# Kernel optimization log

Measured on AMD Instinct MI355X. Metric: run time of the kernel, lower is better.

Reference implementation:

```python
import jax, jax.numpy as jnp
import numpy as np

# ---- architecture constants ----
SENSOR = 128          # u feature width
B_LAYERS = 5          # branch MLP: 4 tanh hidden + 1 linear out
B_UNITS = 1024
LORA = 64
TU = 128              # trunk hidden units
TL = 4                # trunk dense layers
TRUNK_DIMS = [1] + [TU] * (TL - 1) + [1]   # 1 -> 128 -> 128 -> 128 -> 1
NO_TRUNK_PARAMS = sum(d_out + d_in * d_out for d_in, d_out in zip(TRUNK_DIMS[:-1], TRUNK_DIMS[1:]))  # 33409
T0, TFINAL = 0.0, 1.0
BATCH = 2048


def setup_inputs() -> dict:
    key = jax.random.key(0)
    ks = jax.random.split(key, 16)
    def glorot(k, shape):
        fan_in, fan_out = shape[0], shape[1]
        s = jnp.sqrt(2.0 / (fan_in + fan_out)).astype(jnp.float32)
        return jax.random.normal(k, shape, dtype=jnp.float32) * s
    inp = {
        "t": jax.random.uniform(ks[0], (BATCH, 1), dtype=jnp.float32),
        "u": jax.random.normal(ks[1], (BATCH, SENSOR), dtype=jnp.float32),
        # branch MLP: Dense(1024)+tanh x4, then Dense(1024)
        "bw0": glorot(ks[2], (SENSOR, B_UNITS)), "bb0": jnp.zeros((B_UNITS,), jnp.float32),
        "bw1": glorot(ks[3], (B_UNITS, B_UNITS)), "bb1": jnp.zeros((B_UNITS,), jnp.float32),
        "bw2": glorot(ks[4], (B_UNITS, B_UNITS)), "bb2": jnp.zeros((B_UNITS,), jnp.float32),
        "bw3": glorot(ks[5], (B_UNITS, B_UNITS)), "bb3": jnp.zeros((B_UNITS,), jnp.float32),
        "bw4": glorot(ks[6], (B_UNITS, B_UNITS)), "bb4": jnp.zeros((B_UNITS,), jnp.float32),
        # LoRA factors generating trunk params
        "W1": glorot(ks[7], (B_UNITS, LORA)),
        "W2": glorot(ks[8], (LORA, NO_TRUNK_PARAMS)),
    }
    return inp


def _slice_trunk(p):
    """Split per-sample flat trunk params [B,P] into (kernel,bias) per layer.
    Flax tree_flatten order per Dense: bias then kernel."""
    layers = []
    k = 0
    for d_in, d_out in zip(TRUNK_DIMS[:-1], TRUNK_DIMS[1:]):
        b = p[:, k:k + d_out]; k += d_out
        W = p[:, k:k + d_in * d_out].reshape(-1, d_in, d_out); k += d_in * d_out
        layers.append((W, b))
    return layers


def reference(t, u, bw0, bb0, bw1, bb1, bw2, bb2, bw3, bb3, bw4, bb4, W1, W2):
    q0 = u[:, :1]                                     # [B,1]
    # branch MLP (hypernetwork body)
    net = u
    for W, b in ((bw0, bb0), (bw1, bb1), (bw2, bb2), (bw3, bb3)):
        net = jnp.tanh(net @ W + b)
    net = net @ bw4 + bb4                             # [B, units]
    # LoRA-generated per-sample trunk params
    params = net @ (W1 @ W2)                          # [B, NO_TRUNK_PARAMS]
    # batched per-sample trunk MLP on t[i] (vectorized form of the Python loop)
    x = t                                             # [B,1]
    trunk_layers = _slice_trunk(params)
    for i, (W, b) in enumerate(trunk_layers):
        x = jnp.einsum('bi,bio->bo', x, W) + b
        if i < TL - 1:
            x = jnp.tanh(x)
    q = x                                             # [B,1]
    # hard constraint: u0 + (t-t0)/(tfinal-t0)*nn
    out = q0 + (t - T0) / (TFINAL - T0) * q           # [B,1]
    return out.reshape(-1)
```

## Files before the change

### kernel.cpp

```cpp
#include <hip/hip_runtime.h>
#include <hip/hip_bf16.h>
#include <stdint.h>

typedef unsigned short u16;
typedef unsigned int   u32;
typedef short s16x8 __attribute__((ext_vector_type(8)));
typedef float f32x4 __attribute__((ext_vector_type(4)));

#define LDP 33409

__device__ __forceinline__ u16 f2bf(float f) {
    union { float f; u32 u; } v; v.f = f;
    u32 r = v.u + 0x7fffu + ((v.u >> 16) & 1u);
    return (u16)(r >> 16);
}
__device__ __forceinline__ float bf2f(u16 h) {
    union { u32 u; float f; } v; v.u = ((u32)h) << 16;
    return v.f;
}
__device__ __forceinline__ float fast_tanh(float x) {
    float e = __expf(2.0f * x);
    return 1.0f - 2.0f / (e + 1.0f);
}
__device__ __forceinline__ f32x4 MFMA(s16x8 a, s16x8 b, f32x4 c) {
    return __builtin_amdgcn_mfma_f32_16x16x32_bf16(a, b, c, 0, 0, 0);
}
__device__ __forceinline__ void gload_lds16(const void* g, void* l) {
    __builtin_amdgcn_global_load_lds(
        (const __attribute__((address_space(1))) u32*)(uintptr_t)g,
        (__attribute__((address_space(3))) u32*)(uintptr_t)l, 16, 0, 0);
}

__global__ __launch_bounds__(256)
void prep0(const float* __restrict__ u, const float* __restrict__ bw0,
           u16* __restrict__ ubf, u16* __restrict__ bw0t)
{
    __shared__ float tile[64][65];
    const int bid = blockIdx.x, tid = threadIdx.x;
    if (bid < 128) {
        int i = (bid * 256 + tid) * 8;
        float4 a = *(const float4*)&u[i];
        float4 b = *(const float4*)&u[i + 4];
        uint4 o;
        o.x = (u32)f2bf(a.x) | ((u32)f2bf(a.y) << 16);
        o.y = (u32)f2bf(a.z) | ((u32)f2bf(a.w) << 16);
        o.z = (u32)f2bf(b.x) | ((u32)f2bf(b.y) << 16);
        o.w = (u32)f2bf(b.z) | ((u32)f2bf(b.w) << 16);
        *(uint4*)&ubf[i] = o;
        return;
    }
    const int idx = bid - 128;
    const int rb = (idx >> 4) * 64, cb = (idx & 15) * 64;
    for (int i = tid; i < 64 * 64; i += 256) {
        int r = i >> 6, c = i & 63;
        tile[r][c] = bw0[(size_t)(rb + r) * 1024 + cb + c];
    }
    __syncthreads();
    for (int i = tid; i < 64 * 64; i += 256) {
        int c = i >> 6, r = i & 63;
        bw0t[(size_t)(cb + c) * 128 + rb + r] = f2bf(tile[r][c]);
    }
}

__global__ __launch_bounds__(256, 2)
void gemm_fused(const u16* __restrict__ A, int lda,
                const u16* __restrict__ Bt, int ldb,
                const float* __restrict__ bias,
                u16* __restrict__ Cout, int ldc, int K, int mode,
                const float* __restrict__ xsrc, u16* __restrict__ xdst,
                const float* __restrict__ bw4, const float* __restrict__ bb4,
                const float* __restrict__ W1, u16* __restrict__ BWt,
                float* __restrict__ bz,
                const float* __restrict__ W2, u16* __restrict__ Btb)
{
    __shared__ __align__(16) char lds[16640];
    const int bid = blockIdx.x, tid = threadIdx.x;

    if (bid < 512) {
        u16 (*As)[64 * 32] = (u16(*)[64 * 32])lds;
        u16 (*Bs)[64 * 32] = (u16(*)[64 * 32])(lds + 8192);
        const int lane = tid & 63, wid = tid >> 6;
        const int wr = wid >> 1, wc = wid & 1;
        const int bn = (bid & 15) * 64, bm = (bid >> 4) * 64;
        const int NT = K >> 5;
        const int arow = tid >> 2, ck = tid & 3;
        const u16* aSrc = A + (size_t)(bm + arow) * lda + (ck ^ (arow & 3)) * 8;
        const u16* bSrc = Bt + (size_t)(bn + arow) * ldb + (ck ^ (arow & 3)) * 8;
        f32x4 acc[2][2] = {};

        auto STAGE = [&](int buf, int t) {
            const int k0 = t << 5;
            gload_lds16(aSrc + k0, (char*)As[buf] + wid * 1024);
            gload_lds16(bSrc + k0, (char*)Bs[buf] + wid * 1024);
        };
        auto COMPUTE = [&](int buf) {
            s16x8 a[2], b[2];
            #pragma unroll
            for (int mi = 0; mi < 2; ++mi) {
                int row = wr * 32 + mi * 16 + (lane & 15);
                int s = (lane >> 4) ^ (row & 3);
                a[mi] = *(const s16x8*)&As[buf][row * 32 + s * 8];
            }
            #pragma unroll
            for (int ni = 0; ni < 2; ++ni) {
                int n = wc * 32 + ni * 16 + (lane & 15);
                int s = (lane >> 4) ^ (n & 3);
                b[ni] = *(const s16x8*)&Bs[buf][n * 32 + s * 8];
            }
            #pragma unroll
            for (int mi = 0; mi < 2; ++mi)
            #pragma unroll
            for (int ni = 0; ni < 2; ++ni)
                acc[mi][ni] = MFMA(a[mi], b[ni], acc[mi][ni]);
        };

        STAGE(0, 0);
        __syncthreads();
        for (int t = 0; t < NT; ++t) {
            if (t + 1 < NT) STAGE((t + 1) & 1, t + 1);
            COMPUTE(t & 1);
            __syncthreads();
        }
        #pragma unroll
        for (int mi = 0; mi < 2; ++mi)
        #pragma unroll
        for (int ni = 0; ni < 2; ++ni) {
            const int col = bn + wc * 32 + ni * 16 + (lane & 15);
            const float bv = bias[col];
            #pragma unroll
            for (int jj = 0; jj < 4; ++jj) {
                const int row = bm + wr * 32 + mi * 16 + (lane >> 4) * 4 + jj;
                Cout[(size_t)row * ldc + col] = f2bf(fast_tanh(acc[mi][ni][jj] + bv));
            }
        }
    } else if (mode <= 2 && bid < 768) {
        float (*tile)[65] = (float(*)[65])lds;
        const int idx = bid - 512;
        const int rb = (idx >> 4) * 64, cb = (idx & 15) * 64;
        for (int i = tid; i < 64 * 64; i += 256) {
            int r = i >> 6, c = i & 63;
            tile[r][c] = xsrc[(size_t)(rb + r) * 1024 + cb + c];
        }
        __syncthreads();
        for (int i = tid; i < 64 * 64; i += 256) {
            int c = i >> 6, r = i & 63;
            xdst[(size_t)(cb + c) * 1024 + rb + r] = f2bf(tile[r][c]);
        }
    } else if (mode == 2) {
        const int lb = bid - 768;
        const int n = tid & 63, jc = tid >> 6;
        if (lb == 512) {
            float (*sh1)[64] = (float(*)[64])lds;
            float a = 0.f;
            for (int j = jc * 256; j < jc * 256 + 256; ++j)
                a = fmaf(bb4[j], W1[j * 64 + n], a);
            sh1[jc][n] = a;
            __syncthreads();
            if (tid < 64)
                bz[tid] = sh1[0][tid] + sh1[1][tid] + sh1[2][tid] + sh1[3][tid];
            return;
        }
        float (*sh)[2][64] = (float(*)[2][64])lds;
        const int k0 = lb * 2;
        float a0 = 0.f, a1 = 0.f;
        for (int j = jc * 256; j < jc * 256 + 256; ++j) {
            float w = W1[j * 64 + n];
            a0 = fmaf(bw4[(size_t)k0 * 1024 + j], w, a0);
            a1 = fmaf(bw4[(size_t)(k0 + 1) * 1024 + j], w, a1);
        }
        sh[jc][0][n] = a0; sh[jc][1][n] = a1;
        __syncthreads();
        if (tid < 128) {
            int kk = tid >> 6, nn = tid & 63;
            float s = sh[0][kk][nn] + sh[1][kk][nn] + sh[2][kk][nn] + sh[3][kk][nn];
            BWt[(size_t)nn * 1024 + k0 + kk] = f2bf(s);
        }
    } else {
        float (*tile)[130] = (float(*)[130])lds;
        const int idx = bid - 512;
        const int layer = idx / 258, pbi = idx % 258;
        u16* Btd = Btb + (size_t)layer * 128 * 8256;
        const int colbase = layer ? 16896 : 384, biasbase = layer ? 16768 : 256;
        const int pb = pbi * 32;
        for (int i = tid; i < 32 * 128; i += 256) {
            int p = pb + (i >> 7), n = i & 127;
            float v = (p < 8192)
                ? W2[(size_t)(p & 63) * LDP + colbase + (size_t)(p >> 6) * 128 + n]
                : W2[(size_t)(p - 8192) * LDP + biasbase + n];
            tile[i >> 7][n] = v;
        }
        __syncthreads();
        for (int i = tid; i < 32 * 128; i += 256) {
            int n = i >> 5, dp = i & 31;
            Btd[(size_t)n * 8256 + pb + dp] = f2bf(tile[dp][n]);
        }
    }
}

__global__ __launch_bounds__(256, 2)
void zgemm(const u16* __restrict__ A, const u16* __restrict__ Bt,
           float* __restrict__ zc)
{
    __shared__ __align__(16) u16 As[2][64 * 32];
    __shared__ __align__(16) u16 Bs[2][64 * 32];
    const int tid = threadIdx.x, lane = tid & 63, wid = tid >> 6;
    const int wr = wid >> 1, wc = wid & 1;
    const int bm = blockIdx.y * 64, kz = blockIdx.z;
    const int t0 = kz * 4, nt = 4;
    const int arow = tid >> 2, ck = tid & 3;
    const u16* aSrc = A + (size_t)(bm + arow) * 1024 + (ck ^ (arow & 3)) * 8;
    const u16* bSrc = Bt + (size_t)arow * 1024 + (ck ^ (arow & 3)) * 8;
    f32x4 acc[2][2] = {};

    auto STAGE = [&](int buf, int t) {
        const int k0 = t << 5;
        gload_lds16(aSrc + k0, (char*)As[buf] + wid * 1024);
        gload_lds16(bSrc + k0, (char*)Bs[buf] + wid * 1024);
    };
    auto COMPUTE = [&](int buf) {
        s16x8 a[2];
        #pragma unroll
        for (int mi = 0; mi < 2; ++mi) {
            int row = wr * 32 + mi * 16 + (lane & 15);
            int s = (lane >> 4) ^ (row & 3);
            a[mi] = *(const s16x8*)&As[buf][row * 32 + s * 8];
        }
        #pragma unroll
        for (int ni = 0; ni < 2; ++ni) {
            int n = wc * 32 + ni * 16 + (lane & 15);
            int s = (lane >> 4) ^ (n & 3);
            s16x8 b = *(const s16x8*)&Bs[buf][n * 32 + s * 8];
            #pragma unroll
            for (int mi = 0; mi < 2; ++mi)
                acc[mi][ni] = MFMA(a[mi], b, acc[mi][ni]);
        }
    };

    STAGE(0, t0);
    __syncthreads();
    for (int t = 0; t < nt; ++t) {
        if (t + 1 < nt) STAGE((t + 1) & 1, t0 + t + 1);
        COMPUTE(t & 1);
        __syncthreads();
    }
    #pragma unroll
    for (int mi = 0; mi < 2; ++mi)
    #pragma unroll
    for (int ni = 0; ni < 2; ++ni) {
        const int col = wc * 32 + ni * 16 + (lane & 15);
        #pragma unroll
        for (int jj = 0; jj < 4; ++jj) {
            const int row = bm + wr * 32 + mi * 16 + (lane >> 4) * 4 + jj;
            zc[((size_t)kz * 2048 + row) * 64 + col] = acc[mi][ni][jj];
        }
    }
}

__global__ __launch_bounds__(256)
void z_l1_h1(const float* __restrict__ zc, const float* __restrict__ bz,
             const float* __restrict__ W2, const float* __restrict__ t,
             u16* __restrict__ z, u16* __restrict__ h1)
{
    __shared__ float zsh[16][64];
    const int rb = blockIdx.x * 16;
    #pragma unroll
    for (int ii = 0; ii < 4; ++ii) {
        int e = ii * 256 + threadIdx.x;
        int r = e >> 6, k = e & 63;
        size_t off = (size_t)(rb + r) * 64 + k;
        float s = bz[k];
        #pragma unroll
        for (int sk = 0; sk < 8; ++sk) s += zc[(size_t)sk * 2048 * 64 + off];
        zsh[r][k] = s;
        z[off] = f2bf(s);
    }
    __syncthreads();
    const int o = threadIdx.x & 127;
    const int rh = (threadIdx.x >> 7) * 8;
    float acc_a[8] = {}, acc_b[8] = {};
    for (int k = 0; k < 64; ++k) {
        float wa = W2[(size_t)k * LDP + o];
        float wb = W2[(size_t)k * LDP + 128 + o];
        #pragma unroll
        for (int r = 0; r < 8; ++r) {
            float zv = zsh[rh + r][k];
            acc_a[r] = fmaf(zv, wa, acc_a[r]);
            acc_b[r] = fmaf(zv, wb, acc_b[r]);
        }
    }
    #pragma unroll
    for (int r = 0; r < 8; ++r) {
        int b = rb + rh + r;
        h1[b * 128 + o] = f2bf(fast_tanh(t[b] * acc_b[r] + acc_a[r]));
    }
}

__global__ __launch_bounds__(512, 2)
void trunk128(const u16* __restrict__ h, const u16* __restrict__ z,
              const u16* __restrict__ Bt, float* __restrict__ Cp)
{
    constexpr int NT = 258, SKT = 16;
    __shared__ __align__(16) u16 As[2][128 * 32];
    __shared__ __align__(16) u16 Bs[2][128 * 32];
    const int tid = threadIdx.x, lane = tid & 63, wid = tid >> 6;
    const int wr = wid >> 1, wc = wid & 1;
    const int bm = blockIdx.x * 128, kz = blockIdx.y;
    const int t0 = (NT * kz) / SKT, t1 = (NT * (kz + 1)) / SKT;
    const int arow = tid >> 2, ck = tid & 3;
    const int b = bm + arow;
    const s16x8 zlo = *(const s16x8*)&z[b * 64 + ck * 8];
    const s16x8 zhi = *(const s16x8*)&z[b * 64 + 32 + ck * 8];
    const int slot = (ck ^ (arow & 3)) * 8;
    f32x4 acc[2][4] = {};

    auto STAGE = [&](int buf, int t) {
        const int p0 = t << 5;
        gload_lds16(Bt + (size_t)arow * 8256 + p0 + (ck ^ (arow & 3)) * 8,
                    (char*)Bs[buf] + wid * 1024);
        const s16x8 zv = (p0 & 32) ? zhi : zlo;
        u16 o8[8];
        if (p0 < 8192) {
            const float hf = bf2f(h[b * 128 + (p0 >> 6)]);
            #pragma unroll
            for (int j = 0; j < 8; ++j) o8[j] = f2bf(hf * bf2f((u16)zv[j]));
        } else {
            #pragma unroll
            for (int j = 0; j < 8; ++j) o8[j] = (u16)zv[j];
        }
        *(s16x8*)&As[buf][arow * 32 + slot] = *(s16x8*)o8;
    };
    auto COMPUTE = [&](int buf) {
        s16x8 a[2], bb[4];
        #pragma unroll
        for (int mi = 0; mi < 2; ++mi) {
            int row = wr * 32 + mi * 16 + (lane & 15);
            int s = (lane >> 4) ^ (row & 3);
            a[mi] = *(const s16x8*)&As[buf][row * 32 + s * 8];
        }
        #pragma unroll
        for (int ni = 0; ni < 4; ++ni) {
            int n = wc * 64 + ni * 16 + (lane & 15);
            int s = (lane >> 4) ^ (n & 3);
            bb[ni] = *(const s16x8*)&Bs[buf][n * 32 + s * 8];
        }
        #pragma unroll
        for (int mi = 0; mi < 2; ++mi)
        #pragma unroll
        for (int ni = 0; ni < 4; ++ni)
            acc[mi][ni] = MFMA(a[mi], bb[ni], acc[mi][ni]);
    };

    STAGE(0, t0);
    __syncthreads();
    const int nt = t1 - t0;
    for (int t = 0; t < nt; ++t) {
        if (t + 1 < nt) STAGE((t + 1) & 1, t0 + t + 1);
        COMPUTE(t & 1);
        __syncthreads();
    }

    #pragma unroll
    for (int mi = 0; mi < 2; ++mi)
    #pragma unroll
    for (int ni = 0; ni < 4; ++ni) {
        const int col = wc * 64 + ni * 16 + (lane & 15);
        #pragma unroll
        for (int jj = 0; jj < 4; ++jj) {
            const int row = bm + wr * 32 + mi * 16 + (lane >> 4) * 4 + jj;
            Cp[((size_t)kz * 2048 + row) * 128 + col] = acc[mi][ni][jj];
        }
    }
}

__global__ __launch_bounds__(256)
void reduce_tanh(const float* __restrict__ Cp, u16* __restrict__ hout) {
    const int idx = blockIdx.x * 256 + threadIdx.x;
    const size_t S = (size_t)2048 * 128;
    float s = 0.f;
    #pragma unroll
    for (int k = 0; k < 16; ++k) s += Cp[idx + k * S];
    hout[idx] = f2bf(fast_tanh(s));
}

__global__ __launch_bounds__(256)
void reduce_out(const float* __restrict__ Cp, const u16* __restrict__ z,
                const float* __restrict__ W2, const float* __restrict__ t,
                const float* __restrict__ u, float* __restrict__ out)
{
    __shared__ float sh[4][128];
    const int wv = threadIdx.x >> 6, l = threadIdx.x & 63;
    const int b = blockIdx.x * 4 + wv;
    const size_t S = (size_t)2048 * 128;
    #pragma unroll
    for (int e = l; e < 128; e += 64) {
        float s = 0.f;
        #pragma unroll
        for (int k = 0; k < 16; ++k) s += Cp[k * S + (size_t)b * 128 + e];
        sh[wv][e] = fast_tanh(s);
    }
    __syncthreads();
    const float* wrow = &W2[(size_t)l * LDP + 33280];
    float acc = wrow[0];
    #pragma unroll 8
    for (int i = 0; i < 128; ++i) acc = fmaf(sh[wv][i], wrow[1 + i], acc);
    float p = bf2f(z[b * 64 + l]) * acc;
    #pragma unroll
    for (int off = 32; off > 0; off >>= 1) p += __shfl_down(p, off);
    if (l == 0) out[b] = u[b * 128] + t[b] * p;
}

extern "C" void kernel_launch(void* const* d_in, const int* in_sizes, int n_in,
                              void* d_out, int out_size, void* d_ws, size_t ws_size,
                              hipStream_t stream)
{
    const float* t   = (const float*)d_in[0];
    const float* u   = (const float*)d_in[1];
    const float* bw0 = (const float*)d_in[2];
    const float* bb0 = (const float*)d_in[3];
    const float* bw1 = (const float*)d_in[4];
    const float* bb1 = (const float*)d_in[5];
    const float* bw2 = (const float*)d_in[6];
    const float* bb2 = (const float*)d_in[7];
    const float* bw3 = (const float*)d_in[8];
    const float* bb3 = (const float*)d_in[9];
    const float* bw4 = (const float*)d_in[10];
    const float* bb4 = (const float*)d_in[11];
    const float* W1  = (const float*)d_in[12];
    const float* W2  = (const float*)d_in[13];
    float* out = (float*)d_out;

    char* base = (char*)d_ws;
    u16*   bw1t = (u16*)(base);
    u16*   bw2t = (u16*)(base + 2097152);
    u16*   bw3t = (u16*)(base + 4194304);
    u16*   actA = (u16*)(base + 6291456);
    u16*   actB = (u16*)(base + 10485760);
    u16*   ubf  = (u16*)(base + 14680064);
    u16*   bw0t = (u16*)(base + 15204352);
    u16*   BWt  = (u16*)(base + 15499264);
    float* bz   = (float*)(base + 15630336);
    u16*   z    = (u16*)(base + 16777216);
    u16*   h1   = (u16*)(base + 17039360);
    u16*   h2   = (u16*)(base + 17563648);
    u16*   Bt   = (u16*)(base + 18087936);
    float* zc = (float*)(base);
    float* Cp = (float*)(base);

    dim3 blk(256);
    prep0<<<160, blk, 0, stream>>>(u, bw0, ubf, bw0t);

    gemm_fused<<<768, blk, 0, stream>>>(
        ubf, 128, bw0t, 128, bb0, actA, 1024, 128, 0,
        bw1, bw1t, bw4, bb4, W1, BWt, bz, W2, Bt);
    gemm_fused<<<768, blk, 0, stream>>>(
        actA, 1024, bw1t, 1024, bb1, actB, 1024, 1024, 1,
        bw2, bw2t, bw4, bb4, W1, BWt, bz, W2, Bt);
    gemm_fused<<<1281, blk, 0, stream>>>(
        actB, 1024, bw2t, 1024, bb2, actA, 1024, 1024, 2,
        bw3, bw3t, bw4, bb4, W1, BWt, bz, W2, Bt);
    gemm_fused<<<1028, blk, 0, stream>>>(
        actA, 1024, bw3t, 1024, bb3, actB, 1024, 1024, 3,
        nullptr, nullptr, bw4, bb4, W1, BWt, bz, W2, Bt);
    zgemm<<<dim3(1, 32, 8), blk, 0, stream>>>(actB, BWt, zc);
    z_l1_h1<<<128, blk, 0, stream>>>(zc, bz, W2, t, z, h1);
    trunk128<<<dim3(16, 16), dim3(512), 0, stream>>>(h1, z, Bt, Cp);
    reduce_tanh<<<1024, blk, 0, stream>>>(Cp, h2);
    trunk128<<<dim3(16, 16), dim3(512), 0, stream>>>(h2, z, Bt + (size_t)128 * 8256, Cp);
    reduce_out<<<512, blk, 0, stream>>>(Cp, z, W2, t, u, out);
}
```

Before: 138.5 us.

## Fuse all stages into one cooperative persistent kernel with grid syncs

Replaces the chain of ten kernel launches with a single cooperative kernel of 256 blocks of 512 threads. All prep, branch GEMM, z-GEMM, trunk and reduction stages run in it, separated by grid.sync(). Weight prep work (transposes, BW and Bt construction) moves to an up-front phase instead of riding alongside the branch GEMMs. Branch GEMM tiles change to 64x128 per block. The aim is to remove launch gaps and tail effects. In exchange, each grid barrier costs time, prep is no longer overlapped with compute, and only 256 blocks stay resident, which may reduce parallelism in the GEMMs.

```diff
diff --git a/kernel.cpp b/kernel.cpp
--- a/kernel.cpp
+++ b/kernel.cpp
@@ -1,6 +1,9 @@
 #include <hip/hip_runtime.h>
+#include <hip/hip_cooperative_groups.h>
 #include <hip/hip_bf16.h>
 #include <stdint.h>
+
+namespace cg = cooperative_groups;
 
 typedef unsigned short u16;
 typedef unsigned int   u32;
@@ -31,215 +34,62 @@
         (__attribute__((address_space(3))) u32*)(uintptr_t)l, 16, 0, 0);
 }
 
-__global__ __launch_bounds__(256)
-void prep0(const float* __restrict__ u, const float* __restrict__ bw0,
-           u16* __restrict__ ubf, u16* __restrict__ bw0t)
+struct Args {
+    const float *t, *u, *bw0, *bb0, *bw1, *bb1, *bw2, *bb2, *bw3, *bb3, *bw4, *bb4, *W1, *W2;
+    float* out;
+    u16 *ubf, *bw0t, *bw1t, *bw2t, *bw3t, *BWt, *z, *h1, *h2, *Bt, *actA, *actB;
+    float *bz, *zc, *Cp;
+};
+
+__device__ __forceinline__ void branch_stage(char* lds,
+        const u16* __restrict__ A, int lda,
+        const u16* __restrict__ Bt, int ldb,
+        const float* __restrict__ bias,
+        u16* __restrict__ C, int K, int bid, int tid)
 {
-    __shared__ float tile[64][65];
-    const int bid = blockIdx.x, tid = threadIdx.x;
-    if (bid < 128) {
-        int i = (bid * 256 + tid) * 8;
-        float4 a = *(const float4*)&u[i];
-        float4 b = *(const float4*)&u[i + 4];
-        uint4 o;
-        o.x = (u32)f2bf(a.x) | ((u32)f2bf(a.y) << 16);
-        o.y = (u32)f2bf(a.z) | ((u32)f2bf(a.w) << 16);
-        o.z = (u32)f2bf(b.x) | ((u32)f2bf(b.y) << 16);
-        o.w = (u32)f2bf(b.z) | ((u32)f2bf(b.w) << 16);
-        *(uint4*)&ubf[i] = o;
-        return;
-    }
-    const int idx = bid - 128;
-    const int rb = (idx >> 4) * 64, cb = (idx & 15) * 64;
-    for (int i = tid; i < 64 * 64; i += 256) {
-        int r = i >> 6, c = i & 63;
-        tile[r][c] = bw0[(size_t)(rb + r) * 1024 + cb + c];
-    }
-    __syncthreads();
-    for (int i = tid; i < 64 * 64; i += 256) {
-        int c = i >> 6, r = i & 63;
-        bw0t[(size_t)(cb + c) * 128 + rb + r] = f2bf(tile[r][c]);
-    }
-}
-
-__global__ __launch_bounds__(256, 2)
-void gemm_fused(const u16* __restrict__ A, int lda,
-                const u16* __restrict__ Bt, int ldb,
-                const float* __restrict__ bias,
-                u16* __restrict__ Cout, int ldc, int K, int mode,
-                const float* __restrict__ xsrc, u16* __restrict__ xdst,
-                const float* __restrict__ bw4, const float* __restrict__ bb4,
-                const float* __restrict__ W1, u16* __restrict__ BWt,
-                float* __restrict__ bz,
-                const float* __restrict__ W2, u16* __restrict__ Btb)
-{
-    __shared__ __align__(16) char lds[16640];
-    const int bid = blockIdx.x, tid = threadIdx.x;
-
-    if (bid < 512) {
-        u16 (*As)[64 * 32] = (u16(*)[64 * 32])lds;
-        u16 (*Bs)[64 * 32] = (u16(*)[64 * 32])(lds + 8192);
-        const int lane = tid & 63, wid = tid >> 6;
-        const int wr = wid >> 1, wc = wid & 1;
-        const int bn = (bid & 15) * 64, bm = (bid >> 4) * 64;
-        const int NT = K >> 5;
-        const int arow = tid >> 2, ck = tid & 3;
-        const u16* aSrc = A + (size_t)(bm + arow) * lda + (ck ^ (arow & 3)) * 8;
-        const u16* bSrc = Bt + (size_t)(bn + arow) * ldb + (ck ^ (arow & 3)) * 8;
-        f32x4 acc[2][2] = {};
-
-        auto STAGE = [&](int buf, int t) {
-            const int k0 = t << 5;
-            gload_lds16(aSrc + k0, (char*)As[buf] + wid * 1024);
-            gload_lds16(bSrc + k0, (char*)Bs[buf] + wid * 1024);
-        };
-        auto COMPUTE = [&](int buf) {
-            s16x8 a[2], b[2];
-            #pragma unroll
-            for (int mi = 0; mi < 2; ++mi) {
-                int row = wr * 32 + mi * 16 + (lane & 15);
-                int s = (lane >> 4) ^ (row & 3);
-                a[mi] = *(const s16x8*)&As[buf][row * 32 + s * 8];
-            }
-            #pragma unroll
-            for (int ni = 0; ni < 2; ++ni) {
-                int n = wc * 32 + ni * 16 + (lane & 15);
-                int s = (lane >> 4) ^ (n & 3);
-                b[ni] = *(const s16x8*)&Bs[buf][n * 32 + s * 8];
-            }
-            #pragma unroll
-            for (int mi = 0; mi < 2; ++mi)
-            #pragma unroll
-            for (int ni = 0; ni < 2; ++ni)
-                acc[mi][ni] = MFMA(a[mi], b[ni], acc[mi][ni]);
-        };
-
-        STAGE(0, 0);
-        __syncthreads();
-        for (int t = 0; t < NT; ++t) {
-            if (t + 1 < NT) STAGE((t + 1) & 1, t + 1);
-            COMPUTE(t & 1);
-            __syncthreads();
-        }
-        #pragma unroll
-        for (int mi = 0; mi < 2; ++mi)
-        #pragma unroll
-        for (int ni = 0; ni < 2; ++ni) {
-            const int col = bn + wc * 32 + ni * 16 + (lane & 15);
-            const float bv = bias[col];
-            #pragma unroll
-            for (int jj = 0; jj < 4; ++jj) {
-                const int row = bm + wr * 32 + mi * 16 + (lane >> 4) * 4 + jj;
-                Cout[(size_t)row * ldc + col] = f2bf(fast_tanh(acc[mi][ni][jj] + bv));
-            }
-        }
-    } else if (mode <= 2 && bid < 768) {
-        float (*tile)[65] = (float(*)[65])lds;
-        const int idx = bid - 512;
-        const int rb = (idx >> 4) * 64, cb = (idx & 15) * 64;
-        for (int i = tid; i < 64 * 64; i += 256) {
-            int r = i >> 6, c = i & 63;
-            tile[r][c] = xsrc[(size_t)(rb + r) * 1024 + cb + c];
-        }
-        __syncthreads();
-        for (int i = tid; i < 64 * 64; i += 256) {
-            int c = i >> 6, r = i & 63;
-            xdst[(size_t)(cb + c) * 1024 + rb + r] = f2bf(tile[r][c]);
-        }
-    } else if (mode == 2) {
-        const int lb = bid - 768;
-        const int n = tid & 63, jc = tid >> 6;
-        if (lb == 512) {
-            float (*sh1)[64] = (float(*)[64])lds;
-            float a = 0.f;
-            for (int j = jc * 256; j < jc * 256 + 256; ++j)
-                a = fmaf(bb4[j], W1[j * 64 + n], a);
-            sh1[jc][n] = a;
-            __syncthreads();
-            if (tid < 64)
-                bz[tid] = sh1[0][tid] + sh1[1][tid] + sh1[2][tid] + sh1[3][tid];
-            return;
-        }
-        float (*sh)[2][64] = (float(*)[2][64])lds;
-        const int k0 = lb * 2;
-        float a0 = 0.f, a1 = 0.f;
-        for (int j = jc * 256; j < jc * 256 + 256; ++j) {
-            float w = W1[j * 64 + n];
-            a0 = fmaf(bw4[(size_t)k0 * 1024 + j], w, a0);
-            a1 = fmaf(bw4[(size_t)(k0 + 1) * 1024 + j], w, a1);
-        }
-        sh[jc][0][n] = a0; sh[jc][1][n] = a1;
-        __syncthreads();
-        if (tid < 128) {
-            int kk = tid >> 6, nn = tid & 63;
-            float s = sh[0][kk][nn] + sh[1][kk][nn] + sh[2][kk][nn] + sh[3][kk][nn];
-            BWt[(size_t)nn * 1024 + k0 + kk] = f2bf(s);
-        }
-    } else {
-        float (*tile)[130] = (float(*)[130])lds;
-        const int idx = bid - 512;
-        const int layer = idx / 258, pbi = idx % 258;
-        u16* Btd = Btb + (size_t)layer * 128 * 8256;
-        const int colbase = layer ? 16896 : 384, biasbase = layer ? 16768 : 256;
-        const int pb = pbi * 32;
-        for (int i = tid; i < 32 * 128; i += 256) {
-            int p = pb + (i >> 7), n = i & 127;
-            float v = (p < 8192)
-                ? W2[(size_t)(p & 63) * LDP + colbase + (size_t)(p >> 6) * 128 + n]
-                : W2[(size_t)(p - 8192) * LDP + biasbase + n];
-            tile[i >> 7][n] = v;
-        }
-        __syncthreads();
-        for (int i = tid; i < 32 * 128; i += 256) {
-            int n = i >> 5, dp = i & 31;
-            Btd[(size_t)n * 8256 + pb + dp] = f2bf(tile[dp][n]);
-        }
-    }
-}
-
-__global__ __launch_bounds__(256, 2)
-void zgemm(const u16* __restrict__ A, const u16* __restrict__ Bt,
-           float* __restrict__ zc)
-{
-    __shared__ __align__(16) u16 As[2][64 * 32];
-    __shared__ __align__(16) u16 Bs[2][64 * 32];
-    const int tid = threadIdx.x, lane = tid & 63, wid = tid >> 6;
-    const int wr = wid >> 1, wc = wid & 1;
-    const int bm = blockIdx.y * 64, kz = blockIdx.z;
-    const int t0 = kz * 4, nt = 4;
-    const int arow = tid >> 2, ck = tid & 3;
-    const u16* aSrc = A + (size_t)(bm + arow) * 1024 + (ck ^ (arow & 3)) * 8;
-    const u16* bSrc = Bt + (size_t)arow * 1024 + (ck ^ (arow & 3)) * 8;
+    u16 (*As)[64 * 32] = (u16(*)[64 * 32])lds;
+    u16 (*Bs)[128 * 32] = (u16(*)[128 * 32])(lds + 8192);
+    const int lane = tid & 63, wid = tid >> 6;
+    const int wr = wid >> 2, wc = wid & 3;
+    const int bn = (bid & 7) * 128, bm = (bid >> 3) * 64;
+    const int NT = K >> 5;
+    const int ck = tid & 3;
+    const int arow = (tid & 255) >> 2;
+    const int brow = tid >> 2;
+    const u16* aSrc = A + (size_t)(bm + arow) * lda + (ck ^ (arow & 3)) * 8;
+    const u16* bSrc = Bt + (size_t)(bn + brow) * ldb + (ck ^ (brow & 3)) * 8;
     f32x4 acc[2][2] = {};
 
     auto STAGE = [&](int buf, int t) {
         const int k0 = t << 5;
-        gload_lds16(aSrc + k0, (char*)As[buf] + wid * 1024);
+        if (tid < 256) gload_lds16(aSrc + k0, (char*)As[buf] + wid * 1024);
         gload_lds16(bSrc + k0, (char*)Bs[buf] + wid * 1024);
     };
     auto COMPUTE = [&](int buf) {
-        s16x8 a[2];
+        s16x8 av[2], bv[2];
         #pragma unroll
         for (int mi = 0; mi < 2; ++mi) {
             int row = wr * 32 + mi * 16 + (lane & 15);
             int s = (lane >> 4) ^ (row & 3);
-            a[mi] = *(const s16x8*)&As[buf][row * 32 + s * 8];
+            av[mi] = *(const s16x8*)&As[buf][row * 32 + s * 8];
         }
         #pragma unroll
         for (int ni = 0; ni < 2; ++ni) {
-            int n = wc * 32 + ni * 16 + (lane & 15);
-            int s = (lane >> 4) ^ (n & 3);
-            s16x8 b = *(const s16x8*)&Bs[buf][n * 32 + s * 8];
-            #pragma unroll
-            for (int mi = 0; mi < 2; ++mi)
-                acc[mi][ni] = MFMA(a[mi], b, acc[mi][ni]);
-        }
-    };
-
-    STAGE(0, t0);
+            int col = wc * 32 + ni * 16 + (lane & 15);
+            int s = (lane >> 4) ^ (col & 3);
+            bv[ni] = *(const s16x8*)&Bs[buf][col * 32 + s * 8];
+        }
+        #pragma unroll
+        for (int mi = 0; mi < 2; ++mi)
+        #pragma unroll
+        for (int ni = 0; ni < 2; ++ni)
+            acc[mi][ni] = MFMA(av[mi], bv[ni], acc[mi][ni]);
+    };
+
+    STAGE(0, 0);
     __syncthreads();
-    for (int t = 0; t < nt; ++t) {
-        if (t + 1 < nt) STAGE((t + 1) & 1, t0 + t + 1);
+    for (int t = 0; t < NT; ++t) {
+        if (t + 1 < NT) STAGE((t + 1) & 1, t + 1);
         COMPUTE(t & 1);
         __syncthreads();
     }
@@ -247,64 +97,77 @@
     for (int mi = 0; mi < 2; ++mi)
     #pragma unroll
     for (int ni = 0; ni < 2; ++ni) {
-        const int col = wc * 32 + ni * 16 + (lane & 15);
+        const int col = bn + wc * 32 + ni * 16 + (lane & 15);
+        const float bvs = bias[col];
         #pragma unroll
         for (int jj = 0; jj < 4; ++jj) {
             const int row = bm + wr * 32 + mi * 16 + (lane >> 4) * 4 + jj;
-            zc[((size_t)kz * 2048 + row) * 64 + col] = acc[mi][ni][jj];
-        }
-    }
-}
-
-__global__ __launch_bounds__(256)
-void z_l1_h1(const float* __restrict__ zc, const float* __restrict__ bz,
-             const float* __restrict__ W2, const float* __restrict__ t,
-             u16* __restrict__ z, u16* __restrict__ h1)
+            C[(size_t)row * 1024 + col] = f2bf(fast_tanh(acc[mi][ni][jj] + bvs));
+        }
+    }
+}
+
+__device__ __forceinline__ void z_stage(char* lds, const u16* __restrict__ actB,
+        const u16* __restrict__ BWt, float* __restrict__ zc, int bid, int tid)
 {
-    __shared__ float zsh[16][64];
-    const int rb = blockIdx.x * 16;
+    u16 (*As)[64 * 32] = (u16(*)[64 * 32])lds;
+    u16 (*Bs)[64 * 32] = (u16(*)[64 * 32])(lds + 8192);
+    const int lane = tid & 63, wid = tid >> 6;
+    const int wr = wid >> 1, wc = wid & 1;
+    const int bm = (bid >> 3) * 64, kz = bid & 7;
+    const int t0 = kz * 4;
+    const int ck = tid & 3;
+    const int arow = (tid & 255) >> 2;
+    const u16* aSrc = actB + (size_t)(bm + arow) * 1024 + (ck ^ (arow & 3)) * 8;
+    const u16* bSrc = BWt + (size_t)arow * 1024 + (ck ^ (arow & 3)) * 8;
+    f32x4 acc[2] = {};
+
+    auto STAGE = [&](int buf, int t) {
+        const int k0 = t << 5;
+        if (tid < 256) gload_lds16(aSrc + k0, (char*)As[buf] + wid * 1024);
+        else           gload_lds16(bSrc + k0, (char*)Bs[buf] + (wid - 4) * 1024);
+    };
+    auto COMPUTE = [&](int buf) {
+        int row = wr * 16 + (lane & 15);
+        int sa = (lane >> 4) ^ (row & 3);
+        s16x8 av = *(const s16x8*)&As[buf][row * 32 + sa * 8];
+        #pragma unroll
+        for (int ni = 0; ni < 2; ++ni) {
+            int col = wc * 32 + ni * 16 + (lane & 15);
+            int sb = (lane >> 4) ^ (col & 3);
+            s16x8 bv = *(const s16x8*)&Bs[buf][col * 32 + sb * 8];
+            acc[ni] = MFMA(av, bv, acc[ni]);
+        }
+    };
+
+    STAGE(0, t0);
+    __syncthreads();
+    for (int t = 0; t < 4; ++t) {
+        if (t + 1 < 4) STAGE((t + 1) & 1, t0 + t + 1);
+        COMPUTE(t & 1);
+        __syncthreads();
+    }
     #pragma unroll
-    for (int ii = 0; ii < 4; ++ii) {
-        int e = ii * 256 + threadIdx.x;
-        int r = e >> 6, k = e & 63;
-        size_t off = (size_t)(rb + r) * 64 + k;
-        float s = bz[k];
-        #pragma unroll
-        for (int sk = 0; sk < 8; ++sk) s += zc[(size_t)sk * 2048 * 64 + off];
-        zsh[r][k] = s;
-        z[off] = f2bf(s);
-    }
-    __syncthreads();
-    const int o = threadIdx.x & 127;
-    const int rh = (threadIdx.x >> 7) * 8;
-    float acc_a[8] = {}, acc_b[8] = {};
-    for (int k = 0; k < 64; ++k) {
-        float wa = W2[(size_t)k * LDP + o];
-        float wb = W2[(size_t)k * LDP + 128 + o];
-        #pragma unroll
-        for (int r = 0; r < 8; ++r) {
-            float zv = zsh[rh + r][k];
-            acc_a[r] = fmaf(zv, wa, acc_a[r]);
-            acc_b[r] = fmaf(zv, wb, acc_b[r]);
-        }
-    }
-    #pragma unroll
-    for (int r = 0; r < 8; ++r) {
-        int b = rb + rh + r;
-        h1[b * 128 + o] = f2bf(fast_tanh(t[b] * acc_b[r] + acc_a[r]));
-    }
-}
-
-__global__ __launch_bounds__(512, 2)
-void trunk128(const u16* __restrict__ h, const u16* __restrict__ z,
-              const u16* __restrict__ Bt, float* __restrict__ Cp)
+    for (int ni = 0; ni < 2; ++ni) {
+        int col = wc * 32 + ni * 16 + (lane & 15);
+        #pragma unroll
+        for (int jj = 0; jj < 4; ++jj) {
+            int row = bm + wr * 16 + (lane >> 4) * 4 + jj;
+            zc[((size_t)kz * 2048 + row) * 64 + col] = acc[ni][jj];
+        }
+    }
+}
+
+__device__ __forceinline__ void trunk_stage(char* lds, const u16* __restrict__ h,
+        const u16* __restrict__ z, const u16* __restrict__ Bt,
+        float* __restrict__ Cp, int bid, int tid)
 {
     constexpr int NT = 258, SKT = 16;
-    __shared__ __align__(16) u16 As[2][128 * 32];
-    __shared__ __align__(16) u16 Bs[2][128 * 32];
-    const int tid = threadIdx.x, lane = tid & 63, wid = tid >> 6;
+    u16 (*As)[128 * 32] = (u16(*)[128 * 32])lds;
+    u16 (*Bs)[128 * 32] = (u16(*)[128 * 32])(lds + 16384);
+    const int lane = tid & 63, wid = tid >> 6;
     const int wr = wid >> 1, wc = wid & 1;
-    const int bm = blockIdx.x * 128, kz = blockIdx.y;
+    const int bm = (bid >> 4) * 128, kz = bid & 15;
     const int t0 = (NT * kz) / SKT, t1 = (NT * (kz + 1)) / SKT;
     const int arow = tid >> 2, ck = tid & 3;
     const int b = bm + arow;
@@ -330,12 +193,12 @@
         *(s16x8*)&As[buf][arow * 32 + slot] = *(s16x8*)o8;
     };
     auto COMPUTE = [&](int buf) {
-        s16x8 a[2], bb[4];
+        s16x8 av[2], bb[4];
         #pragma unroll
         for (int mi = 0; mi < 2; ++mi) {
             int row = wr * 32 + mi * 16 + (lane & 15);
             int s = (lane >> 4) ^ (row & 3);
-            a[mi] = *(const s16x8*)&As[buf][row * 32 + s * 8];
+            av[mi] = *(const s16x8*)&As[buf][row * 32 + s * 8];
         }
         #pragma unroll
         for (int ni = 0; ni < 4; ++ni) {
@@ -347,7 +210,7 @@
         for (int mi = 0; mi < 2; ++mi)
         #pragma unroll
         for (int ni = 0; ni < 4; ++ni)
-            acc[mi][ni] = MFMA(a[mi], bb[ni], acc[mi][ni]);
+            acc[mi][ni] = MFMA(av[mi], bb[ni], acc[mi][ni]);
     };
 
     STAGE(0, t0);
@@ -358,7 +221,6 @@
         COMPUTE(t & 1);
         __syncthreads();
     }
-
     #pragma unroll
     for (int mi = 0; mi < 2; ++mi)
     #pragma unroll
@@ -372,99 +234,231 @@
     }
 }
 
-__global__ __launch_bounds__(256)
-void reduce_tanh(const float* __restrict__ Cp, u16* __restrict__ hout) {
-    const int idx = blockIdx.x * 256 + threadIdx.x;
-    const size_t S = (size_t)2048 * 128;
-    float s = 0.f;
-    #pragma unroll
-    for (int k = 0; k < 16; ++k) s += Cp[idx + k * S];
-    hout[idx] = f2bf(fast_tanh(s));
-}
-
-__global__ __launch_bounds__(256)
-void reduce_out(const float* __restrict__ Cp, const u16* __restrict__ z,
-                const float* __restrict__ W2, const float* __restrict__ t,
-                const float* __restrict__ u, float* __restrict__ out)
+__global__ __launch_bounds__(512, 2)
+void mega(Args a)
 {
-    __shared__ float sh[4][128];
-    const int wv = threadIdx.x >> 6, l = threadIdx.x & 63;
-    const int b = blockIdx.x * 4 + wv;
-    const size_t S = (size_t)2048 * 128;
-    #pragma unroll
-    for (int e = l; e < 128; e += 64) {
-        float s = 0.f;
-        #pragma unroll
-        for (int k = 0; k < 16; ++k) s += Cp[k * S + (size_t)b * 128 + e];
-        sh[wv][e] = fast_tanh(s);
-    }
-    __syncthreads();
-    const float* wrow = &W2[(size_t)l * LDP + 33280];
-    float acc = wrow[0];
-    #pragma unroll 8
-    for (int i = 0; i < 128; ++i) acc = fmaf(sh[wv][i], wrow[1 + i], acc);
-    float p = bf2f(z[b * 64 + l]) * acc;
-    #pragma unroll
-    for (int off = 32; off > 0; off >>= 1) p += __shfl_down(p, off);
-    if (l == 0) out[b] = u[b * 128] + t[b] * p;
+    __shared__ __align__(16) char lds[32768];
+    cg::grid_group grid = cg::this_grid();
+    const int bid = blockIdx.x, tid = threadIdx.x;
+
+    for (int unit = bid; unit < 1893; unit += 256) {
+        __syncthreads();
+        if (unit < 64) {
+            int i = (unit * 512 + tid) * 8;
+            float4 x = *(const float4*)&a.u[i];
+            float4 y = *(const float4*)&a.u[i + 4];
+            uint4 o;
+            o.x = (u32)f2bf(x.x) | ((u32)f2bf(x.y) << 16);
+            o.y = (u32)f2bf(x.z) | ((u32)f2bf(x.w) << 16);
+            o.z = (u32)f2bf(y.x) | ((u32)f2bf(y.y) << 16);
+            o.w = (u32)f2bf(y.z) | ((u32)f2bf(y.w) << 16);
+            *(uint4*)&a.ubf[i] = o;
+        } else if (unit < 864) {
+            float (*tile)[65] = (float(*)[65])lds;
+            const float* src; u16* dst; int lddst, rb, cb;
+            if (unit < 96) {
+                int idx = unit - 64;
+                src = a.bw0; dst = a.bw0t; lddst = 128;
+                rb = (idx >> 4) * 64; cb = (idx & 15) * 64;
+            } else {
+                int idx = unit - 96;
+                int ly = idx >> 8, w = idx & 255;
+                src = ly == 0 ? a.bw1 : (ly == 1 ? a.bw2 : a.bw3);
+                dst = ly == 0 ? a.bw1t : (ly == 1 ? a.bw2t : a.bw3t);
+                lddst = 1024;
+                rb = (w >> 4) * 64; cb = (w & 15) * 64;
+            }
+            for (int i = tid; i < 4096; i += 512) {
+                int r = i >> 6, c = i & 63;
+                tile[r][c] = src[(size_t)(rb + r) * 1024 + cb + c];
+            }
+            __syncthreads();
+            for (int i = tid; i < 4096; i += 512) {
+                int c = i >> 6, r = i & 63;
+                dst[(size_t)(cb + c) * lddst + rb + r] = f2bf(tile[r][c]);
+            }
+        } else if (unit < 1376) {
+            float (*sh)[2][64] = (float(*)[2][64])lds;
+            const int k0 = (unit - 864) * 2;
+            const int n = tid & 63, jc = tid >> 6;
+            float a0 = 0.f, a1 = 0.f;
+            for (int j = jc * 128; j < jc * 128 + 128; ++j) {
+                float w = a.W1[j * 64 + n];
+                a0 = fmaf(a.bw4[(size_t)k0 * 1024 + j], w, a0);
+                a1 = fmaf(a.bw4[(size_t)(k0 + 1) * 1024 + j], w, a1);
+            }
+            sh[jc][0][n] = a0; sh[jc][1][n] = a1;
+            __syncthreads();
+            if (tid < 128) {
+                int kk = tid >> 6, nn = tid & 63;
+                float s = 0.f;
+                #pragma unroll
+                for (int q = 0; q < 8; ++q) s += sh[q][kk][nn];
+                a.BWt[(size_t)nn * 1024 + k0 + kk] = f2bf(s);
+            }
+        } else if (unit == 1376) {
+            float (*sh1)[64] = (float(*)[64])lds;
+            const int n = tid & 63, jc = tid >> 6;
+            float s = 0.f;
+            for (int j = jc * 128; j < jc * 128 + 128; ++j)
+                s = fmaf(a.bb4[j], a.W1[j * 64 + n], s);
+            sh1[jc][n] = s;
+            __syncthreads();
+            if (tid < 64) {
+                float v = 0.f;
+                #pragma unroll
+                for (int q = 0; q < 8; ++q) v += sh1[q][tid];
+                a.bz[tid] = v;
+            }
+        } else {
+            float (*tile)[130] = (float(*)[130])lds;
+            const int idx = unit - 1377;
+            const int ly = idx / 258, pbi = idx % 258;
+            u16* Btd = a.Bt + (size_t)ly * 128 * 8256;
+            const int colbase = ly ? 16896 : 384, biasbase = ly ? 16768 : 256;
+            const int pb = pbi * 32;
+            for (int i = tid; i < 4096; i += 512) {
+                int p = pb + (i >> 7), n = i & 127;
+                float v = (p < 8192)
+                    ? a.W2[(size_t)(p & 63) * LDP + colbase + (size_t)(p >> 6) * 128 + n]
+                    : a.W2[(size_t)(p - 8192) * LDP + biasbase + n];
+                tile[i >> 7][n] = v;
+            }
+            __syncthreads();
+            for (int i = tid; i < 4096; i += 512) {
+                int n = i >> 5, dp = i & 31;
+                Btd[(size_t)n * 8256 + pb + dp] = f2bf(tile[dp][n]);
+            }
+        }
+    }
+    grid.sync();
+
+    branch_stage(lds, a.ubf, 128, a.bw0t, 128, a.bb0, a.actA, 128, bid, tid);
+    grid.sync();
+    branch_stage(lds, a.actA, 1024, a.bw1t, 1024, a.bb1, a.actB, 1024, bid, tid);
+    grid.sync();
+    branch_stage(lds, a.actB, 1024, a.bw2t, 1024, a.bb2, a.actA, 1024, bid, tid);
+    grid.sync();
+    branch_stage(lds, a.actA, 1024, a.bw3t, 1024, a.bb3, a.actB, 1024, bid, tid);
+    grid.sync();
+
+    z_stage(lds, a.actB, a.BWt, a.zc, bid, tid);
+    grid.sync();
+
+    {
+        float (*zsh)[64] = (float(*)[64])lds;
+        const int rb = bid * 8;
+        {
+            int r = tid >> 6, k = tid & 63;
+            size_t off = (size_t)(rb + r) * 64 + k;
+            float s = a.bz[k];
+            #pragma unroll
+            for (int sk = 0; sk < 8; ++sk) s += a.zc[(size_t)sk * 2048 * 64 + off];
+            zsh[r][k] = s;
+            a.z[off] = f2bf(s);
+        }
+        __syncthreads();
+        const int o = tid & 127;
+        const int rg = (tid >> 7) * 2;
+        float aa[2] = {}, ab[2] = {};
+        for (int k = 0; k < 64; ++k) {
+            float wa = a.W2[(size_t)k * LDP + o];
+            float wb = a.W2[(size_t)k * LDP + 128 + o];
+            #pragma unroll
+            for (int rr = 0; rr < 2; ++rr) {
+                float zv = zsh[rg + rr][k];
+                aa[rr] = fmaf(zv, wa, aa[rr]);
+                ab[rr] = fmaf(zv, wb, ab[rr]);
+            }
+        }
+        #pragma unroll
+        for (int rr = 0; rr < 2; ++rr) {
+            int b = rb + rg + rr;
+            a.h1[b * 128 + o] = f2bf(fast_tanh(a.t[b] * ab[rr] + aa[rr]));
+        }
+    }
+    grid.sync();
+
+    trunk_stage(lds, a.h1, a.z, a.Bt, a.Cp, bid, tid);
+    grid.sync();
+
+    {
+        const size_t S = (size_t)2048 * 128;
+        #pragma unroll
+        for (int q = 0; q < 2; ++q) {
+            int e = bid * 1024 + q * 512 + tid;
+            float s = 0.f;
+            #pragma unroll
+            for (int k = 0; k < 16; ++k) s += a.Cp[e + k * S];
+            a.h2[e] = f2bf(fast_tanh(s));
+        }
+    }
+    grid.sync();
+
+    trunk_stage(lds, a.h2, a.z, a.Bt + (size_t)128 * 8256, a.Cp, bid, tid);
+    grid.sync();
+
+    {
+        float (*sh)[128] = (float(*)[128])lds;
+        const int wv = tid >> 6, l = tid & 63;
+        const int b = bid * 8 + wv;
+        const size_t S = (size_t)2048 * 128;
+        #pragma unroll
+        for (int e = l; e < 128; e += 64) {
+            float s = 0.f;
+            #pragma unroll
+            for (int k = 0; k < 16; ++k) s += a.Cp[k * S + (size_t)b * 128 + e];
+            sh[wv][e] = fast_tanh(s);
+        }
+        __syncthreads();
+        const float* wrow = &a.W2[(size_t)l * LDP + 33280];
+        float acc = wrow[0];
+        #pragma unroll 8
+        for (int i = 0; i < 128; ++i) acc = fmaf(sh[wv][i], wrow[1 + i], acc);
+        float p = bf2f(a.z[b * 64 + l]) * acc;
+        #pragma unroll
+        for (int off = 32; off > 0; off >>= 1) p += __shfl_down(p, off);
+        if (l == 0) a.out[b] = a.u[b * 128] + a.t[b] * p;
+    }
 }
 
 extern "C" void kernel_launch(void* const* d_in, const int* in_sizes, int n_in,
                               void* d_out, int out_size, void* d_ws, size_t ws_size,
                               hipStream_t stream)
 {
-    const float* t   = (const float*)d_in[0];
-    const float* u   = (const float*)d_in[1];
-    const float* bw0 = (const float*)d_in[2];
-    const float* bb0 = (const float*)d_in[3];
-    const float* bw1 = (const float*)d_in[4];
-    const float* bb1 = (const float*)d_in[5];
-    const float* bw2 = (const float*)d_in[6];
-    const float* bb2 = (const float*)d_in[7];
-    const float* bw3 = (const float*)d_in[8];
-    const float* bb3 = (const float*)d_in[9];
-    const float* bw4 = (const float*)d_in[10];
-    const float* bb4 = (const float*)d_in[11];
-    const float* W1  = (const float*)d_in[12];
-    const float* W2  = (const float*)d_in[13];
-    float* out = (float*)d_out;
-
     char* base = (char*)d_ws;
-    u16*   bw1t = (u16*)(base);
-    u16*   bw2t = (u16*)(base + 2097152);
-    u16*   bw3t = (u16*)(base + 4194304);
-    u16*   actA = (u16*)(base + 6291456);
-    u16*   actB = (u16*)(base + 10485760);
-    u16*   ubf  = (u16*)(base + 14680064);
-    u16*   bw0t = (u16*)(base + 15204352);
-    u16*   BWt  = (u16*)(base + 15499264);
-    float* bz   = (float*)(base + 15630336);
-    u16*   z    = (u16*)(base + 16777216);
-    u16*   h1   = (u16*)(base + 17039360);
-    u16*   h2   = (u16*)(base + 17563648);
-    u16*   Bt   = (u16*)(base + 18087936);
-    float* zc = (float*)(base);
-    float* Cp = (float*)(base);
-
-    dim3 blk(256);
-    prep0<<<160, blk, 0, stream>>>(u, bw0, ubf, bw0t);
-
-    gemm_fused<<<768, blk, 0, stream>>>(
-        ubf, 128, bw0t, 128, bb0, actA, 1024, 128, 0,
-        bw1, bw1t, bw4, bb4, W1, BWt, bz, W2, Bt);
-    gemm_fused<<<768, blk, 0, stream>>>(
-        actA, 1024, bw1t, 1024, bb1, actB, 1024, 1024, 1,
-        bw2, bw2t, bw4, bb4, W1, BWt, bz, W2, Bt);
-    gemm_fused<<<1281, blk, 0, stream>>>(
-        actB, 1024, bw2t, 1024, bb2, actA, 1024, 1024, 2,
-        bw3, bw3t, bw4, bb4, W1, BWt, bz, W2, Bt);
-    gemm_fused<<<1028, blk, 0, stream>>>(
-        actA, 1024, bw3t, 1024, bb3, actB, 1024, 1024, 3,
-        nullptr, nullptr, bw4, bb4, W1, BWt, bz, W2, Bt);
-    zgemm<<<dim3(1, 32, 8), blk, 0, stream>>>(actB, BWt, zc);
-    z_l1_h1<<<128, blk, 0, stream>>>(zc, bz, W2, t, z, h1);
-    trunk128<<<dim3(16, 16), dim3(512), 0, stream>>>(h1, z, Bt, Cp);
-    reduce_tanh<<<1024, blk, 0, stream>>>(Cp, h2);
-    trunk128<<<dim3(16, 16), dim3(512), 0, stream>>>(h2, z, Bt + (size_t)128 * 8256, Cp);
-    reduce_out<<<512, blk, 0, stream>>>(Cp, z, W2, t, u, out);
-}
+    Args a;
+    a.t   = (const float*)d_in[0];
+    a.u   = (const float*)d_in[1];
+    a.bw0 = (const float*)d_in[2];
+    a.bb0 = (const float*)d_in[3];
+    a.bw1 = (const float*)d_in[4];
+    a.bb1 = (const float*)d_in[5];
+    a.bw2 = (const float*)d_in[6];
+    a.bb2 = (const float*)d_in[7];
+    a.bw3 = (const float*)d_in[8];
+    a.bb3 = (const float*)d_in[9];
+    a.bw4 = (const float*)d_in[10];
+    a.bb4 = (const float*)d_in[11];
+    a.W1  = (const float*)d_in[12];
+    a.W2  = (const float*)d_in[13];
+    a.out = (float*)d_out;
+    a.bw1t = (u16*)(base);
+    a.bw2t = (u16*)(base + 2097152);
+    a.bw3t = (u16*)(base + 4194304);
+    a.actA = (u16*)(base + 6291456);
+    a.actB = (u16*)(base + 10485760);
+    a.ubf  = (u16*)(base + 14680064);
+    a.bw0t = (u16*)(base + 15204352);
+    a.BWt  = (u16*)(base + 15499264);
+    a.bz   = (float*)(base + 15630336);
+    a.z    = (u16*)(base + 16777216);
+    a.h1   = (u16*)(base + 17039360);
+    a.h2   = (u16*)(base + 17563648);
+    a.Bt   = (u16*)(base + 18087936);
+    a.zc   = (float*)(base);
+    a.Cp   = (float*)(base);
+
+    void* params[] = { (void*)&a };
+    hipLaunchCooperativeKernel((void*)mega, dim3(256), dim3(512), params, 0, stream);
+}
```

Measured after the change: 466.1 us. +236.6%, slower.

## Enlarge branch GEMM tile to 128x64 and vectorize reduce_tanh

Applied to the files above, without the earlier changes.

Each block of the branch-MLP GEMM now computes a 128x64 output tile instead of 64x64, with each wave holding a 4x2 MFMA accumulator grid. This halves the GEMM block count and improves A/B operand reuse per LDS stage. Grid sizes and auxiliary-block offsets are shifted to match. Separately, reduce_tanh processes four elements per thread with float4 loads and packed bf16 stores, using a quarter of the blocks. The larger tile needs more LDS and more registers, and with 256 GEMM blocks the CUs may be less fully occupied.

```diff
diff --git a/kernel.cpp b/kernel.cpp
--- a/kernel.cpp
+++ b/kernel.cpp
@@ -73,45 +73,47 @@
                 float* __restrict__ bz,
                 const float* __restrict__ W2, u16* __restrict__ Btb)
 {
-    __shared__ __align__(16) char lds[16640];
+    __shared__ __align__(16) char lds[24576];
     const int bid = blockIdx.x, tid = threadIdx.x;
 
-    if (bid < 512) {
-        u16 (*As)[64 * 32] = (u16(*)[64 * 32])lds;
-        u16 (*Bs)[64 * 32] = (u16(*)[64 * 32])(lds + 8192);
+    if (bid < 256) {
+        u16 (*As)[128 * 32] = (u16(*)[128 * 32])lds;
+        u16 (*Bs)[64 * 32]  = (u16(*)[64 * 32])(lds + 16384);
         const int lane = tid & 63, wid = tid >> 6;
         const int wr = wid >> 1, wc = wid & 1;
-        const int bn = (bid & 15) * 64, bm = (bid >> 4) * 64;
+        const int bn = (bid & 15) * 64, bm = (bid >> 4) * 128;
         const int NT = K >> 5;
         const int arow = tid >> 2, ck = tid & 3;
         const u16* aSrc = A + (size_t)(bm + arow) * lda + (ck ^ (arow & 3)) * 8;
         const u16* bSrc = Bt + (size_t)(bn + arow) * ldb + (ck ^ (arow & 3)) * 8;
-        f32x4 acc[2][2] = {};
+        const size_t aHalf = (size_t)64 * lda;
+        f32x4 acc[4][2] = {};
 
         auto STAGE = [&](int buf, int t) {
             const int k0 = t << 5;
-            gload_lds16(aSrc + k0, (char*)As[buf] + wid * 1024);
-            gload_lds16(bSrc + k0, (char*)Bs[buf] + wid * 1024);
+            gload_lds16(aSrc + k0,         (char*)As[buf] + wid * 1024);
+            gload_lds16(aSrc + aHalf + k0, (char*)As[buf] + 4096 + wid * 1024);
+            gload_lds16(bSrc + k0,         (char*)Bs[buf] + wid * 1024);
         };
         auto COMPUTE = [&](int buf) {
-            s16x8 a[2], b[2];
-            #pragma unroll
-            for (int mi = 0; mi < 2; ++mi) {
-                int row = wr * 32 + mi * 16 + (lane & 15);
+            s16x8 av[4], bv[2];
+            #pragma unroll
+            for (int mi = 0; mi < 4; ++mi) {
+                int row = wr * 64 + mi * 16 + (lane & 15);
                 int s = (lane >> 4) ^ (row & 3);
-                a[mi] = *(const s16x8*)&As[buf][row * 32 + s * 8];
+                av[mi] = *(const s16x8*)&As[buf][row * 32 + s * 8];
             }
             #pragma unroll
             for (int ni = 0; ni < 2; ++ni) {
-                int n = wc * 32 + ni * 16 + (lane & 15);
-                int s = (lane >> 4) ^ (n & 3);
-                b[ni] = *(const s16x8*)&Bs[buf][n * 32 + s * 8];
+                int col = wc * 32 + ni * 16 + (lane & 15);
+                int s = (lane >> 4) ^ (col & 3);
+                bv[ni] = *(const s16x8*)&Bs[buf][col * 32 + s * 8];
             }
             #pragma unroll
-            for (int mi = 0; mi < 2; ++mi)
+            for (int mi = 0; mi < 4; ++mi)
             #pragma unroll
             for (int ni = 0; ni < 2; ++ni)
-                acc[mi][ni] = MFMA(a[mi], b[ni], acc[mi][ni]);
+                acc[mi][ni] = MFMA(av[mi], bv[ni], acc[mi][ni]);
         };
 
         STAGE(0, 0);
@@ -122,20 +124,20 @@
             __syncthreads();
         }
         #pragma unroll
-        for (int mi = 0; mi < 2; ++mi)
+        for (int mi = 0; mi < 4; ++mi)
         #pragma unroll
         for (int ni = 0; ni < 2; ++ni) {
             const int col = bn + wc * 32 + ni * 16 + (lane & 15);
             const float bv = bias[col];
             #pragma unroll
             for (int jj = 0; jj < 4; ++jj) {
-                const int row = bm + wr * 32 + mi * 16 + (lane >> 4) * 4 + jj;
+                const int row = bm + wr * 64 + mi * 16 + (lane >> 4) * 4 + jj;
                 Cout[(size_t)row * ldc + col] = f2bf(fast_tanh(acc[mi][ni][jj] + bv));
             }
         }
-    } else if (mode <= 2 && bid < 768) {
+    } else if (mode <= 2 && bid < 512) {
         float (*tile)[65] = (float(*)[65])lds;
-        const int idx = bid - 512;
+        const int idx = bid - 256;
         const int rb = (idx >> 4) * 64, cb = (idx & 15) * 64;
         for (int i = tid; i < 64 * 64; i += 256) {
             int r = i >> 6, c = i & 63;
@@ -147,7 +149,7 @@
             xdst[(size_t)(cb + c) * 1024 + rb + r] = f2bf(tile[r][c]);
         }
     } else if (mode == 2) {
-        const int lb = bid - 768;
+        const int lb = bid - 512;
         const int n = tid & 63, jc = tid >> 6;
         if (lb == 512) {
             float (*sh1)[64] = (float(*)[64])lds;
@@ -177,7 +179,7 @@
         }
     } else {
         float (*tile)[130] = (float(*)[130])lds;
-        const int idx = bid - 512;
+        const int idx = bid - 256;
         const int layer = idx / 258, pbi = idx % 258;
         u16* Btd = Btb + (size_t)layer * 128 * 8256;
         const int colbase = layer ? 16896 : 384, biasbase = layer ? 16768 : 256;
@@ -330,12 +332,12 @@
         *(s16x8*)&As[buf][arow * 32 + slot] = *(s16x8*)o8;
     };
     auto COMPUTE = [&](int buf) {
-        s16x8 a[2], bb[4];
+        s16x8 av[2], bb[4];
         #pragma unroll
         for (int mi = 0; mi < 2; ++mi) {
             int row = wr * 32 + mi * 16 + (lane & 15);
             int s = (lane >> 4) ^ (row & 3);
-            a[mi] = *(const s16x8*)&As[buf][row * 32 + s * 8];
+            av[mi] = *(const s16x8*)&As[buf][row * 32 + s * 8];
         }
         #pragma unroll
         for (int ni = 0; ni < 4; ++ni) {
@@ -347,7 +349,7 @@
         for (int mi = 0; mi < 2; ++mi)
         #pragma unroll
         for (int ni = 0; ni < 4; ++ni)
-            acc[mi][ni] = MFMA(a[mi], bb[ni], acc[mi][ni]);
+            acc[mi][ni] = MFMA(av[mi], bb[ni], acc[mi][ni]);
     };
 
     STAGE(0, t0);
@@ -374,12 +376,18 @@
 
 __global__ __launch_bounds__(256)
 void reduce_tanh(const float* __restrict__ Cp, u16* __restrict__ hout) {
-    const int idx = blockIdx.x * 256 + threadIdx.x;
+    const int i4 = (blockIdx.x * 256 + threadIdx.x) * 4;
     const size_t S = (size_t)2048 * 128;
-    float s = 0.f;
-    #pragma unroll
-    for (int k = 0; k < 16; ++k) s += Cp[idx + k * S];
-    hout[idx] = f2bf(fast_tanh(s));
+    float4 s = make_float4(0.f, 0.f, 0.f, 0.f);
+    #pragma unroll
+    for (int k = 0; k < 16; ++k) {
+        float4 v = *(const float4*)&Cp[(size_t)k * S + i4];
+        s.x += v.x; s.y += v.y; s.z += v.z; s.w += v.w;
+    }
+    uint2 o;
+    o.x = (u32)f2bf(fast_tanh(s.x)) | ((u32)f2bf(fast_tanh(s.y)) << 16);
+    o.y = (u32)f2bf(fast_tanh(s.z)) | ((u32)f2bf(fast_tanh(s.w)) << 16);
+    *(uint2*)&hout[i4] = o;
 }
 
 __global__ __launch_bounds__(256)
@@ -449,22 +457,22 @@
     dim3 blk(256);
     prep0<<<160, blk, 0, stream>>>(u, bw0, ubf, bw0t);
 
-    gemm_fused<<<768, blk, 0, stream>>>(
+    gemm_fused<<<512, blk, 0, stream>>>(
         ubf, 128, bw0t, 128, bb0, actA, 1024, 128, 0,
         bw1, bw1t, bw4, bb4, W1, BWt, bz, W2, Bt);
-    gemm_fused<<<768, blk, 0, stream>>>(
+    gemm_fused<<<512, blk, 0, stream>>>(
         actA, 1024, bw1t, 1024, bb1, actB, 1024, 1024, 1,
         bw2, bw2t, bw4, bb4, W1, BWt, bz, W2, Bt);
-    gemm_fused<<<1281, blk, 0, stream>>>(
+    gemm_fused<<<1025, blk, 0, stream>>>(
         actB, 1024, bw2t, 1024, bb2, actA, 1024, 1024, 2,
         bw3, bw3t, bw4, bb4, W1, BWt, bz, W2, Bt);
-    gemm_fused<<<1028, blk, 0, stream>>>(
+    gemm_fused<<<772, blk, 0, stream>>>(
         actA, 1024, bw3t, 1024, bb3, actB, 1024, 1024, 3,
         nullptr, nullptr, bw4, bb4, W1, BWt, bz, W2, Bt);
     zgemm<<<dim3(1, 32, 8), blk, 0, stream>>>(actB, BWt, zc);
     z_l1_h1<<<128, blk, 0, stream>>>(zc, bz, W2, t, z, h1);
     trunk128<<<dim3(16, 16), dim3(512), 0, stream>>>(h1, z, Bt, Cp);
-    reduce_tanh<<<1024, blk, 0, stream>>>(Cp, h2);
+    reduce_tanh<<<256, blk, 0, stream>>>(Cp, h2);
     trunk128<<<dim3(16, 16), dim3(512), 0, stream>>>(h2, z, Bt + (size_t)128 * 8256, Cp);
     reduce_out<<<512, blk, 0, stream>>>(Cp, z, W2, t, u, out);
 }
```

New measurement: 137.9 us. Within noise of the previous version (-0.4%).
